# Kernel tuning notes

Measured on AMD Instinct MI355X. Metric: run time of the kernel, lower is better.

## Reference

```python
import jax, jax.numpy as jnp
import numpy as np

D_MODEL = 1024  # scale uses full model dim, as in the source
MASKED = True


def setup_inputs() -> dict:
    key = jax.random.key(0)
    kq, kk, kv = jax.random.split(key, 3)
    B, H, S, Dh = 4, 16, 2048, 64
    Q = jax.random.normal(kq, (B, H, S, Dh), dtype=jnp.float32)
    K = jax.random.normal(kk, (B, H, S, Dh), dtype=jnp.float32)
    V = jax.random.normal(kv, (B, H, S, Dh), dtype=jnp.float32)
    return {"Q": Q, "K": K, "V": V}


def reference(Q, K, V):
    scale = 1.0 / (D_MODEL ** 0.5)
    # [B,H,Sq,Sk] score matrix
    scores = jnp.einsum('bhqd,bhkd->bhqk', Q, K) * scale
    if MASKED:
        S = Q.shape[-2]
        causal = jnp.tril(jnp.ones((S, S), dtype=bool))  # True on/below diag
        scores = jnp.where(causal, scores, jnp.float32(-jnp.inf))
    probs = jax.nn.softmax(scores, axis=-1)
    return jnp.einsum('bhqk,bhkd->bhqd', probs, V)
```

## Files before the change

kernel.cpp:

```cpp
#include <hip/hip_runtime.h>

typedef _Float16 half2_t __attribute__((ext_vector_type(2)));
typedef _Float16 half4_t __attribute__((ext_vector_type(4)));
typedef _Float16 half8_t __attribute__((ext_vector_type(8)));
typedef float    f32x4   __attribute__((ext_vector_type(4)));
typedef unsigned int u32x4 __attribute__((ext_vector_type(4)));

#define S_LEN 2048
#define DH    64
#define QBLK  128
#define KVB   64
#define NQB   16
#define SCALE 0.045110910340389066f

__device__ __forceinline__ int swz_off(int row, int byteInRow) {
    return row * 128 + (byteInRow ^ ((row & 7) << 4));
}

__device__ __forceinline__ half4_t cvt4(f32x4 x) {
    half2_t a = __builtin_bit_cast(half2_t, __builtin_amdgcn_cvt_pkrtz(x[0], x[1]));
    half2_t b = __builtin_bit_cast(half2_t, __builtin_amdgcn_cvt_pkrtz(x[2], x[3]));
    half4_t r; r[0] = a[0]; r[1] = a[1]; r[2] = b[0]; r[3] = b[1];
    return r;
}
__device__ __forceinline__ unsigned int pk2(float a, float b) {
    return __builtin_bit_cast(unsigned int, __builtin_amdgcn_cvt_pkrtz(a, b));
}

__global__ __launch_bounds__(256, 3)
void fattn_kernel(const float* __restrict__ Qg, const float* __restrict__ Kg,
                  const float* __restrict__ Vg, float* __restrict__ Og) {
    __shared__ __align__(16) char smem[32768];

    const int bh  = (int)blockIdx.x;
    const int qb  = (NQB - 1) - (int)blockIdx.y;
    const int q0  = qb * QBLK;
    const int tid = (int)threadIdx.x;
    const int lane = tid & 63;
    const int w    = tid >> 6;
    const int c    = lane & 15;
    const int g    = lane >> 4;

    const size_t base = (size_t)bh * S_LEN * DH;
    const float* Qp = Qg + base;
    const float* Kp = Kg + base;
    const float* Vp = Vg + base;
    float*       Op = Og + base;

    const int qrow = q0 + w * 32;
    const int nT = 2 * qb + 2;

    const bool isK = tid < 128;
    const int sid = tid & 127;
    const int r0  = sid >> 4;
    const int c4  = (sid & 15) << 2;
    const int kLds0 = swz_off(r0, c4 * 2);
    const int kq4 = (sid >> 4) << 2;
    const int d4  = (sid & 15) << 2;
    const int vb = (kq4 < 16) ? (4 * kq4) : (4 * kq4 - 56);

    half8_t qf[2][2];
#pragma unroll
    for (int qt = 0; qt < 2; ++qt) {
        const float* qptr = Qp + (size_t)(qrow + qt * 16 + c) * DH;
#pragma unroll
        for (int s = 0; s < 2; ++s) {
            f32x4 a = *(const f32x4*)(qptr + s * 32 + g * 8);
            f32x4 b = *(const f32x4*)(qptr + s * 32 + g * 8 + 4);
            half8_t h;
#pragma unroll
            for (int j = 0; j < 4; ++j) {
                h[j]     = (_Float16)(a[j] * SCALE);
                h[j + 4] = (_Float16)(b[j] * SCALE);
            }
            qf[qt][s] = h;
        }
    }

    half8_t ones;
#pragma unroll
    for (int j = 0; j < 8; ++j) ones[j] = (_Float16)1.0f;

    f32x4 oacc0[4], oacc1[4];
#pragma unroll
    for (int dt = 0; dt < 4; ++dt) {
        oacc0[dt] = (f32x4){0.f, 0.f, 0.f, 0.f};
        oacc1[dt] = (f32x4){0.f, 0.f, 0.f, 0.f};
    }
    f32x4 lacc0 = (f32x4){0.f, 0.f, 0.f, 0.f};
    f32x4 lacc1 = (f32x4){0.f, 0.f, 0.f, 0.f};

    f32x4 pr[8];
    auto stage_load = [&](int kv) {
        if (isK) {
#pragma unroll
            for (int i = 0; i < 8; ++i)
                pr[i] = *(const f32x4*)(Kp + (size_t)((kv + r0 + 8 * i) * DH + c4));
        } else {
#pragma unroll
            for (int h = 0; h < 2; ++h)
#pragma unroll
                for (int j = 0; j < 4; ++j)
                    pr[4 * h + j] = *(const f32x4*)(Vp + (size_t)((kv + kq4 + 32 * h + j) * DH + d4));
        }
    };
    auto stage_write = [&](char* buf) {
        if (isK) {
#pragma unroll
            for (int i = 0; i < 8; ++i)
                *(half4_t*)(buf + kLds0 + i * 1024) = cvt4(pr[i]);
        } else {
            char* Vw = buf + 8192;
#pragma unroll
            for (int h = 0; h < 2; ++h)
#pragma unroll
                for (int jj = 0; jj < 4; ++jj) {
                    half2_t lo = __builtin_bit_cast(half2_t, __builtin_amdgcn_cvt_pkrtz(pr[4*h+0][jj], pr[4*h+1][jj]));
                    half2_t hi = __builtin_bit_cast(half2_t, __builtin_amdgcn_cvt_pkrtz(pr[4*h+2][jj], pr[4*h+3][jj]));
                    half4_t col; col[0] = lo[0]; col[1] = lo[1]; col[2] = hi[0]; col[3] = hi[1];
                    *(half4_t*)(Vw + swz_off(d4 + jj, vb + 64 * h)) = col;
                }
        }
    };

    stage_load(0);
    stage_write(smem);

    int cur = 0;
    for (int t = 0; t < nT; ++t) {
        __syncthreads();
        const bool pf = (t + 1 < nT);
        if (pf) stage_load((t + 1) * KVB);

        const int kv0 = t * KVB;
        char* const Ks = smem + cur * 16384;
        char* const Vs = Ks + 8192;

        if (kv0 <= qrow + 31) {
            f32x4 st0[4], st1[4];
#pragma unroll
            for (int kt = 0; kt < 4; ++kt) {
                st0[kt] = (f32x4){0.f, 0.f, 0.f, 0.f};
                st1[kt] = (f32x4){0.f, 0.f, 0.f, 0.f};
            }
            __builtin_amdgcn_s_setprio(1);
#pragma unroll
            for (int kt = 0; kt < 4; ++kt) {
                half8_t kf0 = *(const half8_t*)(Ks + swz_off(kt * 16 + c, g * 16));
                half8_t kf1 = *(const half8_t*)(Ks + swz_off(kt * 16 + c, 64 + g * 16));
                st0[kt] = __builtin_amdgcn_mfma_f32_16x16x32_f16(kf0, qf[0][0], st0[kt], 0, 0, 0);
                st0[kt] = __builtin_amdgcn_mfma_f32_16x16x32_f16(kf1, qf[0][1], st0[kt], 0, 0, 0);
                st1[kt] = __builtin_amdgcn_mfma_f32_16x16x32_f16(kf0, qf[1][0], st1[kt], 0, 0, 0);
                st1[kt] = __builtin_amdgcn_mfma_f32_16x16x32_f16(kf1, qf[1][1], st1[kt], 0, 0, 0);
            }
            __builtin_amdgcn_s_setprio(0);

            if (kv0 + KVB - 1 > qrow) {
                const int qq0 = qrow + c;
                const int qq1 = qrow + 16 + c;
#pragma unroll
                for (int kt = 0; kt < 4; ++kt)
#pragma unroll
                    for (int r = 0; r < 4; ++r) {
                        const int kk = kv0 + kt * 16 + g * 4 + r;
                        if (kk > qq0) st0[kt][r] = -1e30f;
                        if (kk > qq1) st1[kt][r] = -1e30f;
                    }
            }

            unsigned int pw[8];
#pragma unroll
            for (int kt = 0; kt < 4; ++kt) {
#pragma unroll
                for (int r = 0; r < 4; ++r)
                    st0[kt][r] = __builtin_amdgcn_exp2f(st0[kt][r]);
                pw[2 * kt]     = pk2(st0[kt][0], st0[kt][1]);
                pw[2 * kt + 1] = pk2(st0[kt][2], st0[kt][3]);
            }
            const half8_t phA0 = __builtin_bit_cast(half8_t, (u32x4){pw[0], pw[1], pw[2], pw[3]});
            const half8_t phA1 = __builtin_bit_cast(half8_t, (u32x4){pw[4], pw[5], pw[6], pw[7]});
#pragma unroll
            for (int kt = 0; kt < 4; ++kt) {
#pragma unroll
                for (int r = 0; r < 4; ++r)
                    st1[kt][r] = __builtin_amdgcn_exp2f(st1[kt][r]);
                pw[2 * kt]     = pk2(st1[kt][0], st1[kt][1]);
                pw[2 * kt + 1] = pk2(st1[kt][2], st1[kt][3]);
            }
            const half8_t phB0 = __builtin_bit_cast(half8_t, (u32x4){pw[0], pw[1], pw[2], pw[3]});
            const half8_t phB1 = __builtin_bit_cast(half8_t, (u32x4){pw[4], pw[5], pw[6], pw[7]});

            __builtin_amdgcn_s_setprio(1);
#pragma unroll
            for (int dt = 0; dt < 4; ++dt) {
                half8_t vf = *(const half8_t*)(Vs + swz_off(dt * 16 + c, g * 16));
                oacc0[dt] = __builtin_amdgcn_mfma_f32_16x16x32_f16(vf, phA0, oacc0[dt], 0, 0, 0);
                oacc1[dt] = __builtin_amdgcn_mfma_f32_16x16x32_f16(vf, phB0, oacc1[dt], 0, 0, 0);
            }
            lacc0 = __builtin_amdgcn_mfma_f32_16x16x32_f16(ones, phA0, lacc0, 0, 0, 0);
            lacc1 = __builtin_amdgcn_mfma_f32_16x16x32_f16(ones, phB0, lacc1, 0, 0, 0);
#pragma unroll
            for (int dt = 0; dt < 4; ++dt) {
                half8_t vf = *(const half8_t*)(Vs + swz_off(dt * 16 + c, 64 + g * 16));
                oacc0[dt] = __builtin_amdgcn_mfma_f32_16x16x32_f16(vf, phA1, oacc0[dt], 0, 0, 0);
                oacc1[dt] = __builtin_amdgcn_mfma_f32_16x16x32_f16(vf, phB1, oacc1[dt], 0, 0, 0);
            }
            lacc0 = __builtin_amdgcn_mfma_f32_16x16x32_f16(ones, phA1, lacc0, 0, 0, 0);
            lacc1 = __builtin_amdgcn_mfma_f32_16x16x32_f16(ones, phB1, lacc1, 0, 0, 0);
            __builtin_amdgcn_s_setprio(0);
        }

        if (pf) stage_write(smem + (cur ^ 1) * 16384);
        cur ^= 1;
    }

    {
        const float inv = __builtin_amdgcn_rcpf(lacc0[0]);
        float* optr = Op + (size_t)(qrow + c) * DH;
#pragma unroll
        for (int dt = 0; dt < 4; ++dt) {
            f32x4 o = oacc0[dt] * inv;
            *(f32x4*)(optr + dt * 16 + g * 4) = o;
        }
    }
    {
        const float inv = __builtin_amdgcn_rcpf(lacc1[0]);
        float* optr = Op + (size_t)(qrow + 16 + c) * DH;
#pragma unroll
        for (int dt = 0; dt < 4; ++dt) {
            f32x4 o = oacc1[dt] * inv;
            *(f32x4*)(optr + dt * 16 + g * 4) = o;
        }
    }
}

extern "C" void kernel_launch(void* const* d_in, const int* in_sizes, int n_in,
                              void* d_out, int out_size, void* d_ws, size_t ws_size,
                              hipStream_t stream) {
    (void)in_sizes; (void)n_in; (void)out_size; (void)d_ws; (void)ws_size;
    const float* Q = (const float*)d_in[0];
    const float* K = (const float*)d_in[1];
    const float* V = (const float*)d_in[2];
    float* O = (float*)d_out;
    dim3 grid(64, NQB);
    fattn_kernel<<<grid, 256, 0, stream>>>(Q, K, V, O);
}
```

Baseline: 57.18 us.

## Software-pipeline PV matmul one KV tile behind QK matmul

Restructures the KV loop so the P·V MFMAs for the previous tile are issued right after the current tile's QK^T MFMAs. The exp2/packing of the current tile then overlaps with matrix work, and V fragments are preloaded into registers before the buffer is overwritten. The causal skip guard (kv0 <= qrow+31) is removed, so every wave now processes all nT tiles. Fully masked tiles contribute zero probabilities but still cost compute. Extra live registers (vf0/vf1, ph*) may reduce occupancy.

```diff
diff --git a/kernel.cpp b/kernel.cpp
--- a/kernel.cpp
+++ b/kernel.cpp
@@ -90,6 +90,9 @@
     f32x4 lacc0 = (f32x4){0.f, 0.f, 0.f, 0.f};
     f32x4 lacc1 = (f32x4){0.f, 0.f, 0.f, 0.f};
 
+    half8_t phA0, phA1, phB0, phB1;
+    half8_t vf0[4], vf1[4];
+
     f32x4 pr[8];
     auto stage_load = [&](int kv) {
         if (isK) {
@@ -136,83 +139,101 @@
         char* const Ks = smem + cur * 16384;
         char* const Vs = Ks + 8192;
 
-        if (kv0 <= qrow + 31) {
-            f32x4 st0[4], st1[4];
-#pragma unroll
-            for (int kt = 0; kt < 4; ++kt) {
-                st0[kt] = (f32x4){0.f, 0.f, 0.f, 0.f};
-                st1[kt] = (f32x4){0.f, 0.f, 0.f, 0.f};
-            }
-            __builtin_amdgcn_s_setprio(1);
-#pragma unroll
-            for (int kt = 0; kt < 4; ++kt) {
-                half8_t kf0 = *(const half8_t*)(Ks + swz_off(kt * 16 + c, g * 16));
-                half8_t kf1 = *(const half8_t*)(Ks + swz_off(kt * 16 + c, 64 + g * 16));
-                st0[kt] = __builtin_amdgcn_mfma_f32_16x16x32_f16(kf0, qf[0][0], st0[kt], 0, 0, 0);
-                st0[kt] = __builtin_amdgcn_mfma_f32_16x16x32_f16(kf1, qf[0][1], st0[kt], 0, 0, 0);
-                st1[kt] = __builtin_amdgcn_mfma_f32_16x16x32_f16(kf0, qf[1][0], st1[kt], 0, 0, 0);
-                st1[kt] = __builtin_amdgcn_mfma_f32_16x16x32_f16(kf1, qf[1][1], st1[kt], 0, 0, 0);
-            }
-            __builtin_amdgcn_s_setprio(0);
-
-            if (kv0 + KVB - 1 > qrow) {
-                const int qq0 = qrow + c;
-                const int qq1 = qrow + 16 + c;
-#pragma unroll
-                for (int kt = 0; kt < 4; ++kt)
-#pragma unroll
-                    for (int r = 0; r < 4; ++r) {
-                        const int kk = kv0 + kt * 16 + g * 4 + r;
-                        if (kk > qq0) st0[kt][r] = -1e30f;
-                        if (kk > qq1) st1[kt][r] = -1e30f;
-                    }
-            }
-
-            unsigned int pw[8];
-#pragma unroll
-            for (int kt = 0; kt < 4; ++kt) {
-#pragma unroll
-                for (int r = 0; r < 4; ++r)
-                    st0[kt][r] = __builtin_amdgcn_exp2f(st0[kt][r]);
-                pw[2 * kt]     = pk2(st0[kt][0], st0[kt][1]);
-                pw[2 * kt + 1] = pk2(st0[kt][2], st0[kt][3]);
-            }
-            const half8_t phA0 = __builtin_bit_cast(half8_t, (u32x4){pw[0], pw[1], pw[2], pw[3]});
-            const half8_t phA1 = __builtin_bit_cast(half8_t, (u32x4){pw[4], pw[5], pw[6], pw[7]});
-#pragma unroll
-            for (int kt = 0; kt < 4; ++kt) {
-#pragma unroll
-                for (int r = 0; r < 4; ++r)
-                    st1[kt][r] = __builtin_amdgcn_exp2f(st1[kt][r]);
-                pw[2 * kt]     = pk2(st1[kt][0], st1[kt][1]);
-                pw[2 * kt + 1] = pk2(st1[kt][2], st1[kt][3]);
-            }
-            const half8_t phB0 = __builtin_bit_cast(half8_t, (u32x4){pw[0], pw[1], pw[2], pw[3]});
-            const half8_t phB1 = __builtin_bit_cast(half8_t, (u32x4){pw[4], pw[5], pw[6], pw[7]});
-
-            __builtin_amdgcn_s_setprio(1);
+        f32x4 st0[4], st1[4];
+#pragma unroll
+        for (int kt = 0; kt < 4; ++kt) {
+            st0[kt] = (f32x4){0.f, 0.f, 0.f, 0.f};
+            st1[kt] = (f32x4){0.f, 0.f, 0.f, 0.f};
+        }
+        __builtin_amdgcn_s_setprio(1);
+#pragma unroll
+        for (int kt = 0; kt < 4; ++kt) {
+            half8_t kf0 = *(const half8_t*)(Ks + swz_off(kt * 16 + c, g * 16));
+            half8_t kf1 = *(const half8_t*)(Ks + swz_off(kt * 16 + c, 64 + g * 16));
+            st0[kt] = __builtin_amdgcn_mfma_f32_16x16x32_f16(kf0, qf[0][0], st0[kt], 0, 0, 0);
+            st0[kt] = __builtin_amdgcn_mfma_f32_16x16x32_f16(kf1, qf[0][1], st0[kt], 0, 0, 0);
+            st1[kt] = __builtin_amdgcn_mfma_f32_16x16x32_f16(kf0, qf[1][0], st1[kt], 0, 0, 0);
+            st1[kt] = __builtin_amdgcn_mfma_f32_16x16x32_f16(kf1, qf[1][1], st1[kt], 0, 0, 0);
+        }
+        if (t > 0) {
 #pragma unroll
             for (int dt = 0; dt < 4; ++dt) {
-                half8_t vf = *(const half8_t*)(Vs + swz_off(dt * 16 + c, g * 16));
-                oacc0[dt] = __builtin_amdgcn_mfma_f32_16x16x32_f16(vf, phA0, oacc0[dt], 0, 0, 0);
-                oacc1[dt] = __builtin_amdgcn_mfma_f32_16x16x32_f16(vf, phB0, oacc1[dt], 0, 0, 0);
+                oacc0[dt] = __builtin_amdgcn_mfma_f32_16x16x32_f16(vf0[dt], phA0, oacc0[dt], 0, 0, 0);
+                oacc1[dt] = __builtin_amdgcn_mfma_f32_16x16x32_f16(vf0[dt], phB0, oacc1[dt], 0, 0, 0);
             }
             lacc0 = __builtin_amdgcn_mfma_f32_16x16x32_f16(ones, phA0, lacc0, 0, 0, 0);
             lacc1 = __builtin_amdgcn_mfma_f32_16x16x32_f16(ones, phB0, lacc1, 0, 0, 0);
 #pragma unroll
             for (int dt = 0; dt < 4; ++dt) {
-                half8_t vf = *(const half8_t*)(Vs + swz_off(dt * 16 + c, 64 + g * 16));
-                oacc0[dt] = __builtin_amdgcn_mfma_f32_16x16x32_f16(vf, phA1, oacc0[dt], 0, 0, 0);
-                oacc1[dt] = __builtin_amdgcn_mfma_f32_16x16x32_f16(vf, phB1, oacc1[dt], 0, 0, 0);
+                oacc0[dt] = __builtin_amdgcn_mfma_f32_16x16x32_f16(vf1[dt], phA1, oacc0[dt], 0, 0, 0);
+                oacc1[dt] = __builtin_amdgcn_mfma_f32_16x16x32_f16(vf1[dt], phB1, oacc1[dt], 0, 0, 0);
             }
             lacc0 = __builtin_amdgcn_mfma_f32_16x16x32_f16(ones, phA1, lacc0, 0, 0, 0);
             lacc1 = __builtin_amdgcn_mfma_f32_16x16x32_f16(ones, phB1, lacc1, 0, 0, 0);
-            __builtin_amdgcn_s_setprio(0);
-        }
+        }
+        __builtin_amdgcn_s_setprio(0);
+
+#pragma unroll
+        for (int dt = 0; dt < 4; ++dt) {
+            vf0[dt] = *(const half8_t*)(Vs + swz_off(dt * 16 + c, g * 16));
+            vf1[dt] = *(const half8_t*)(Vs + swz_off(dt * 16 + c, 64 + g * 16));
+        }
+
+        if (kv0 + KVB - 1 > qrow) {
+            const int qq0 = qrow + c;
+            const int qq1 = qrow + 16 + c;
+#pragma unroll
+            for (int kt = 0; kt < 4; ++kt)
+#pragma unroll
+                for (int r = 0; r < 4; ++r) {
+                    const int kk = kv0 + kt * 16 + g * 4 + r;
+                    if (kk > qq0) st0[kt][r] = -1e30f;
+                    if (kk > qq1) st1[kt][r] = -1e30f;
+                }
+        }
+
+        unsigned int pw[8];
+#pragma unroll
+        for (int kt = 0; kt < 4; ++kt) {
+#pragma unroll
+            for (int r = 0; r < 4; ++r)
+                st0[kt][r] = __builtin_amdgcn_exp2f(st0[kt][r]);
+            pw[2 * kt]     = pk2(st0[kt][0], st0[kt][1]);
+            pw[2 * kt + 1] = pk2(st0[kt][2], st0[kt][3]);
+        }
+        phA0 = __builtin_bit_cast(half8_t, (u32x4){pw[0], pw[1], pw[2], pw[3]});
+        phA1 = __builtin_bit_cast(half8_t, (u32x4){pw[4], pw[5], pw[6], pw[7]});
+#pragma unroll
+        for (int kt = 0; kt < 4; ++kt) {
+#pragma unroll
+            for (int r = 0; r < 4; ++r)
+                st1[kt][r] = __builtin_amdgcn_exp2f(st1[kt][r]);
+            pw[2 * kt]     = pk2(st1[kt][0], st1[kt][1]);
+            pw[2 * kt + 1] = pk2(st1[kt][2], st1[kt][3]);
+        }
+        phB0 = __builtin_bit_cast(half8_t, (u32x4){pw[0], pw[1], pw[2], pw[3]});
+        phB1 = __builtin_bit_cast(half8_t, (u32x4){pw[4], pw[5], pw[6], pw[7]});
 
         if (pf) stage_write(smem + (cur ^ 1) * 16384);
         cur ^= 1;
     }
+
+    __builtin_amdgcn_s_setprio(1);
+#pragma unroll
+    for (int dt = 0; dt < 4; ++dt) {
+        oacc0[dt] = __builtin_amdgcn_mfma_f32_16x16x32_f16(vf0[dt], phA0, oacc0[dt], 0, 0, 0);
+        oacc1[dt] = __builtin_amdgcn_mfma_f32_16x16x32_f16(vf0[dt], phB0, oacc1[dt], 0, 0, 0);
+    }
+    lacc0 = __builtin_amdgcn_mfma_f32_16x16x32_f16(ones, phA0, lacc0, 0, 0, 0);
+    lacc1 = __builtin_amdgcn_mfma_f32_16x16x32_f16(ones, phB0, lacc1, 0, 0, 0);
+#pragma unroll
+    for (int dt = 0; dt < 4; ++dt) {
+        oacc0[dt] = __builtin_amdgcn_mfma_f32_16x16x32_f16(vf1[dt], phA1, oacc0[dt], 0, 0, 0);
+        oacc1[dt] = __builtin_amdgcn_mfma_f32_16x16x32_f16(vf1[dt], phB1, oacc1[dt], 0, 0, 0);
+    }
+    lacc0 = __builtin_amdgcn_mfma_f32_16x16x32_f16(ones, phA1, lacc0, 0, 0, 0);
+    lacc1 = __builtin_amdgcn_mfma_f32_16x16x32_f16(ones, phB1, lacc1, 0, 0, 0);
+    __builtin_amdgcn_s_setprio(0);
 
     {
         const float inv = __builtin_amdgcn_rcpf(lacc0[0]);
```

After: 186.6 us. 3.26x slower.
